# Optimization experiments

Measured on AMD Instinct MI355X. Metric: run time of the kernel, lower is better.

The kernel has to match this reference:

```python
import jax, jax.numpy as jnp
import numpy as np

H, C = 8, 32          # heads, per-head channels
N, E = 100000, 1600000
NEG_SLOPE = 0.2
LN_EPS = 1e-5


def layer_norm(x, g, b):
    mu = jnp.mean(x, axis=-1, keepdims=True)
    var = jnp.mean((x - mu) ** 2, axis=-1, keepdims=True)
    return (x - mu) * jax.lax.rsqrt(var + LN_EPS) * g + b


def setup_inputs() -> dict:
    key = jax.random.key(0)
    ks = jax.random.split(key, 8)
    x = jax.random.normal(ks[0], (N, C), dtype=jnp.float32)
    edge_index = jax.random.randint(ks[1], (2, E), 0, N, dtype=jnp.int64)
    s = 1.0 / np.sqrt(C)
    W_gat = jax.random.normal(ks[2], (C, H * C), dtype=jnp.float32) * s
    att_src = jax.random.normal(ks[3], (H, C), dtype=jnp.float32) * s
    att_dst = jax.random.normal(ks[4], (H, C), dtype=jnp.float32) * s
    bias_gat = jnp.zeros((C,), jnp.float32)
    w1 = jax.random.normal(ks[5], (C, 128), dtype=jnp.float32) * s
    b1 = jnp.zeros((128,), jnp.float32)
    w2 = jax.random.normal(ks[6], (128, C), dtype=jnp.float32) / np.sqrt(128)
    b2 = jnp.zeros((C,), jnp.float32)
    g1 = jnp.ones((C,), jnp.float32); be1 = jnp.zeros((C,), jnp.float32)
    g2 = jnp.ones((C,), jnp.float32); be2 = jnp.zeros((C,), jnp.float32)
    return dict(x=x, edge_index=edge_index, W_gat=W_gat, att_src=att_src,
                att_dst=att_dst, bias_gat=bias_gat, w1=w1, b1=b1, w2=w2,
                b2=b2, g1=g1, be1=be1, g2=g2, be2=be2)


def gat_conv(x, edge_index, W_gat, att_src, att_dst, bias_gat):
    n = x.shape[0]
    # add self loops (PyG default)
    loops = jnp.arange(n, dtype=edge_index.dtype)
    ei = jnp.concatenate([edge_index, jnp.stack([loops, loops])], axis=1)
    src, dst = ei[0], ei[1]
    xp = (x @ W_gat).reshape(n, H, C)                      # [N,H,C]
    a_src = jnp.einsum('nhc,hc->nh', xp, att_src)          # [N,H]
    a_dst = jnp.einsum('nhc,hc->nh', xp, att_dst)
    alpha = jax.nn.leaky_relu(a_src[src] + a_dst[dst], NEG_SLOPE)  # [E',H]
    # segment softmax over incoming edges of each dst node
    m = jax.ops.segment_max(alpha, dst, num_segments=n)
    ea = jnp.exp(alpha - m[dst])
    denom = jax.ops.segment_sum(ea, dst, num_segments=n)
    attn = ea / (denom[dst] + 1e-16)                       # [E',H]
    msg = xp[src] * attn[..., None]                        # [E',H,C]
    out = jax.ops.segment_sum(msg, dst, num_segments=n)    # [N,H,C]
    return out.mean(axis=1) + bias_gat                     # concat=False -> head mean


def reference(x, edge_index, W_gat, att_src, att_dst, bias_gat,
              w1, b1, w2, b2, g1, be1, g2, be2):
    h = gat_conv(x, edge_index, W_gat, att_src, att_dst, bias_gat)
    h = layer_norm(h + x, g1, be1)
    ff = jax.nn.relu(h @ w1 + b1) @ w2 + b2
    return layer_norm(ff + h, g2, be2)
```

## Files before the change

### kernel.cpp

```cpp
#include <hip/hip_runtime.h>
#include <hip/hip_fp16.h>
#include <stdint.h>

#define HH 8
#define CC 32
#define HC 256
#define FF 128
#define NEG 0.2f
#define LNEPS 1e-5f

typedef __attribute__((ext_vector_type(8))) short bf16x8;
typedef __attribute__((ext_vector_type(4))) float f32x4;
typedef unsigned short u16;

__device__ inline unsigned bf16r(float f) {
  unsigned u = __float_as_uint(f);
  return (u + 0x7fffu + ((u >> 16) & 1u)) >> 16;
}
__device__ inline float bflo(unsigned w) { return __uint_as_float(w << 16); }
__device__ inline float bfhi(unsigned w) { return __uint_as_float(w & 0xffff0000u); }
__device__ inline float leaky(float v) { return v >= 0.f ? v : NEG * v; }
__device__ inline float h2f(unsigned hbits) {
  return __half2float(__ushort_as_half((unsigned short)hbits));
}
__device__ inline u16 f2h(float f) {
  return __half_as_ushort(__float2half(f));
}
__device__ inline float ub0(unsigned w) { return (float)(w & 0xffu); }
__device__ inline float ub1(unsigned w) { return (float)((w >> 8) & 0xffu); }
__device__ inline float ub2(unsigned w) { return (float)((w >> 16) & 0xffu); }
__device__ inline float ub3(unsigned w) { return (float)(w >> 24); }

__global__ __launch_bounds__(256) void klayout(
    const float* __restrict__ W, const float* __restrict__ atts,
    const float* __restrict__ attd, const float* __restrict__ w1,
    const float* __restrict__ w2,
    u16* __restrict__ Wb, u16* __restrict__ Zb,
    u16* __restrict__ V1b, u16* __restrict__ V2b)
{
  int t = threadIdx.x;
  for (int i = t; i < 16 * 512; i += 256) {
    int j = i & 7, l = (i >> 3) & 63, nb = i >> 9;
    int k = 8 * (l >> 4) + j, c = 16 * nb + (l & 15);
    Wb[i] = (u16)bf16r(W[k * HC + c]);
  }
  for (int i = t; i < 8 * 512; i += 256) {
    int j = i & 7, l = (i >> 3) & 63, kb = i >> 9;
    int k = 32 * kb + 8 * (l >> 4) + j;
    int tc = l & 15;
    float v = 0.f;
    if (tc < 8)  { if ((k >> 5) == tc)     v = atts[tc * 32 + (k & 31)]; }
    else         { if ((k >> 5) == tc - 8) v = attd[(tc - 8) * 32 + (k & 31)]; }
    Zb[i] = (u16)bf16r(v);
  }
  for (int i = t; i < 8 * 512; i += 256) {
    int j = i & 7, l = (i >> 3) & 63, nb = i >> 9;
    int k = 8 * (l >> 4) + j, c = 16 * nb + (l & 15);
    V1b[i] = (u16)bf16r(w1[k * FF + c]);
  }
  for (int i = t; i < 8 * 512; i += 256) {
    int j = i & 7, l = (i >> 3) & 63, kn = i >> 9;
    int kb = kn >> 1, nb2 = kn & 1;
    int k = 32 * kb + 8 * (l >> 4) + j, c = 16 * nb2 + (l & 15);
    V2b[i] = (u16)bf16r(w2[k * CC + c]);
  }
}

__global__ __launch_bounds__(256) void khist(
    const int* __restrict__ ei, int e, int n,
    int* __restrict__ deg4, unsigned* __restrict__ dstr)
{
  int r = (int)blockIdx.x & 3;
  int* dr = deg4 + (size_t)r * n;
  int i = (int)blockIdx.x * 1024 + (int)threadIdx.x * 4;
  if (i >= e) return;
  const int* dst = ei + e;
  if (i + 3 < e) {
    int4 d4 = *(const int4*)(dst + i);
    unsigned r0 = (unsigned)atomicAdd(&dr[d4.x], 1);
    unsigned r1 = (unsigned)atomicAdd(&dr[d4.y], 1);
    unsigned r2 = (unsigned)atomicAdd(&dr[d4.z], 1);
    unsigned r3 = (unsigned)atomicAdd(&dr[d4.w], 1);
    uint4 o;
    o.x = (unsigned)d4.x | ((unsigned)r << 17) | (r0 << 19);
    o.y = (unsigned)d4.y | ((unsigned)r << 17) | (r1 << 19);
    o.z = (unsigned)d4.z | ((unsigned)r << 17) | (r2 << 19);
    o.w = (unsigned)d4.w | ((unsigned)r << 17) | (r3 << 19);
    *(uint4*)(dstr + i) = o;
  } else {
    for (int k = 0; k < 4 && i + k < e; ++k) {
      int d = dst[i + k];
      unsigned rr = (unsigned)atomicAdd(&dr[d], 1);
      dstr[i + k] = (unsigned)d | ((unsigned)r << 17) | (rr << 19);
    }
  }
}

__global__ __launch_bounds__(256) void k1c(
    const float* __restrict__ x, const u16* __restrict__ Wb,
    const u16* __restrict__ Zb,
    unsigned* __restrict__ xq8, unsigned* __restrict__ ascp,
    float* __restrict__ a_d, int n)
{
  __shared__ u16 lt[4][16 * 264];
  __shared__ float lsc[4][16][8];
  int wid = threadIdx.x >> 6, lane = threadIdx.x & 63;
  int q = lane & 15, g = lane >> 4;
  long node0 = (long)((int)blockIdx.x * 4 + wid) * 16;
  if (node0 + 16 > n) node0 = n - 16;
  u16* L = lt[wid];

  const float* xr = x + (node0 + q) * CC + 8 * g;
  float4 xa = *(const float4*)xr, xb = *(const float4*)(xr + 4);
  bf16x8 af;
  af[0] = (short)bf16r(xa.x); af[1] = (short)bf16r(xa.y);
  af[2] = (short)bf16r(xa.z); af[3] = (short)bf16r(xa.w);
  af[4] = (short)bf16r(xb.x); af[5] = (short)bf16r(xb.y);
  af[6] = (short)bf16r(xb.z); af[7] = (short)bf16r(xb.w);

#pragma unroll
  for (int nb = 0; nb < 16; ++nb) {
    bf16x8 bf = *(const bf16x8*)(Wb + nb * 512 + lane * 8);
    f32x4 acc = {0.f, 0.f, 0.f, 0.f};
    acc = __builtin_amdgcn_mfma_f32_16x16x32_bf16(af, bf, acc, 0, 0, 0);
    int col = 16 * nb + q;
#pragma unroll
    for (int r = 0; r < 4; ++r)
      L[(4 * g + r) * 264 + col] = (u16)bf16r(acc[r]);
  }
  __syncthreads();

  f32x4 az = {0.f, 0.f, 0.f, 0.f};
#pragma unroll
  for (int kb = 0; kb < 8; ++kb) {
    bf16x8 a2 = *(const bf16x8*)(L + q * 264 + kb * 32 + g * 8);
    bf16x8 zb = *(const bf16x8*)(Zb + kb * 512 + lane * 8);
    az = __builtin_amdgcn_mfma_f32_16x16x32_bf16(a2, zb, az, 0, 0, 0);
  }
  int hq = q & 7;
  u16* ascp16 = (u16*)ascp;
  if (q < 8) {
#pragma unroll
    for (int r = 0; r < 4; ++r)
      ascp16[((node0 + 4 * g + r) * HH + hq) * 2] = (u16)bf16r(az[r]);
  } else {
#pragma unroll
    for (int r = 0; r < 4; ++r)
      a_d[(node0 + 4 * g + r) * HH + hq] = az[r];
  }

#pragma unroll
  for (int t2 = 0; t2 < 2; ++t2) {
    int task = t2 * 64 + lane;
    int r = task >> 3, h = task & 7;
    const unsigned* p = (const unsigned*)(L + r * 264 + h * 32);
    float mx = 0.f;
#pragma unroll
    for (int i = 0; i < 16; ++i) {
      unsigned w = p[i];
      mx = fmaxf(mx, fmaxf(fabsf(bflo(w)), fabsf(bfhi(w))));
    }
    float rinv = (mx > 0.f) ? 127.f / mx : 0.f;
    ascp16[((node0 + r) * HH + h) * 2 + 1] = f2h(mx * (1.f / 127.f));
    lsc[wid][r][h] = rinv;
  }
  __syncthreads();

#pragma unroll
  for (int i = 0; i < 16; ++i) {
    int d = i * 64 + lane;
    int r = d >> 6, c = d & 63;
    int h = c >> 3;
    float rv = lsc[wid][r][h];
    const unsigned* p = (const unsigned*)(L + r * 264) + (c << 1);
    unsigned w0 = p[0], w1 = p[1];
    int q0 = __float2int_rn(bflo(w0) * rv);
    int q1 = __float2int_rn(bfhi(w0) * rv);
    int q2 = __float2int_rn(bflo(w1) * rv);
    int q3 = __float2int_rn(bfhi(w1) * rv);
    q0 = min(max(q0, -127), 127) + 128;
    q1 = min(max(q1, -127), 127) + 128;
    q2 = min(max(q2, -127), 127) + 128;
    q3 = min(max(q3, -127), 127) + 128;
    unsigned pk = (unsigned)q0 | ((unsigned)q1 << 8) |
                  ((unsigned)q2 << 16) | ((unsigned)q3 << 24);
    xq8[(node0 + r) * 64 + c] = pk;
  }
}

__global__ __launch_bounds__(256) void kscanA(const int* __restrict__ deg4,
                                              int* __restrict__ bsum, int n)
{
  __shared__ int ws[4];
  int t = threadIdx.x;
  int i = (int)blockIdx.x * 1024 + t * 4;
  int s = 0;
  if (i + 3 < n) {
#pragma unroll
    for (int r = 0; r < 4; ++r) {
      int4 v = *(const int4*)(deg4 + (size_t)r * n + i);
      s += v.x + v.y + v.z + v.w;
    }
  } else {
    for (int k = 0; k < 4 && i + k < n; ++k)
#pragma unroll
      for (int r = 0; r < 4; ++r) s += deg4[(size_t)r * n + i + k];
  }
#pragma unroll
  for (int mask = 1; mask < 64; mask <<= 1) s += __shfl_xor(s, mask);
  if ((t & 63) == 0) ws[t >> 6] = s;
  __syncthreads();
  if (t == 0) bsum[blockIdx.x] = ws[0] + ws[1] + ws[2] + ws[3];
}

__global__ __launch_bounds__(1024) void kscanB(int* __restrict__ bsum, int nb)
{
  __shared__ int wsum[16];
  int t = threadIdx.x, lane = t & 63, wid = t >> 6;
  int v = (t < nb) ? bsum[t] : 0;
  int s = v;
#pragma unroll
  for (int d = 1; d < 64; d <<= 1) { int tt = __shfl_up(s, d); if (lane >= d) s += tt; }
  if (lane == 63) wsum[wid] = s;
  __syncthreads();
  if (wid == 0) {
    int w = (lane < 16) ? wsum[lane] : 0;
#pragma unroll
    for (int d = 1; d < 16; d <<= 1) { int tt = __shfl_up(w, d); if (lane >= d) w += tt; }
    if (lane < 16) wsum[lane] = w;
  }
  __syncthreads();
  int excl = s - v + ((wid > 0) ? wsum[wid - 1] : 0);
  if (t < nb) bsum[t] = excl;
}

__global__ __launch_bounds__(256) void kscanC(const int* __restrict__ deg4,
                                              const int* __restrict__ bsum,
                                              int* __restrict__ rb,
                                              int* __restrict__ degt, int n)
{
  __shared__ int ws[4];
  int t = threadIdx.x, lane = t & 63, wid = t >> 6;
  int i = (int)blockIdx.x * 1024 + t * 4;
  int c0[4] = {0,0,0,0}, c1[4] = {0,0,0,0}, c2[4] = {0,0,0,0}, c3[4] = {0,0,0,0};
  if (i + 3 < n) {
    int4 v0 = *(const int4*)(deg4 + 0 * (size_t)n + i);
    int4 v1 = *(const int4*)(deg4 + 1 * (size_t)n + i);
    int4 v2 = *(const int4*)(deg4 + 2 * (size_t)n + i);
    int4 v3 = *(const int4*)(deg4 + 3 * (size_t)n + i);
    c0[0]=v0.x;c0[1]=v0.y;c0[2]=v0.z;c0[3]=v0.w;
    c1[0]=v1.x;c1[1]=v1.y;c1[2]=v1.z;c1[3]=v1.w;
    c2[0]=v2.x;c2[1]=v2.y;c2[2]=v2.z;c2[3]=v2.w;
    c3[0]=v3.x;c3[1]=v3.y;c3[2]=v3.z;c3[3]=v3.w;
  } else {
    for (int k = 0; k < 4 && i + k < n; ++k) {
      c0[k] = deg4[0 * (size_t)n + i + k];
      c1[k] = deg4[1 * (size_t)n + i + k];
      c2[k] = deg4[2 * (size_t)n + i + k];
      c3[k] = deg4[3 * (size_t)n + i + k];
    }
  }
  int tot[4];
#pragma unroll
  for (int k = 0; k < 4; ++k) tot[k] = c0[k] + c1[k] + c2[k] + c3[k];
  int tsum = tot[0] + tot[1] + tot[2] + tot[3];
  int s = tsum;
#pragma unroll
  for (int d = 1; d < 64; d <<= 1) { int tt = __shfl_up(s, d); if (lane >= d) s += tt; }
  if (lane == 63) ws[wid] = s;
  __syncthreads();
  if (t == 0) {
    int a = ws[0]; ws[0] = 0;
    int b = ws[1]; ws[1] = a; a += b;
    int c = ws[2]; ws[2] = a; a += c;
    ws[3] = a;
  }
  __syncthreads();
  int base = bsum[blockIdx.x] + ws[wid] + (s - tsum);
#pragma unroll
  for (int k = 0; k < 4; ++k) {
    if (i + k < n) {
      int b0 = base;
      rb[0 * (size_t)n + i + k] = b0;
      rb[1 * (size_t)n + i + k] = b0 + c0[k];
      rb[2 * (size_t)n + i + k] = b0 + c0[k] + c1[k];
      rb[3 * (size_t)n + i + k] = b0 + c0[k] + c1[k] + c2[k];
      degt[i + k] = tot[k];
    }
    base += tot[k];
  }
}

__global__ __launch_bounds__(256) void kscatter(
    const int* __restrict__ ei, const unsigned* __restrict__ dstr, int e,
    const int* __restrict__ rb, int* __restrict__ csr, int n)
{
  int oct = (int)blockIdx.x & 3;
  int nsub = (int)gridDim.x >> 2;
  int sub = (int)blockIdx.x >> 2;
  int nper = (n + 3) >> 2;
  int lo = oct * nper, hi = lo + nper;
  int stride = nsub << 10;
  for (int i = (sub * 256 + (int)threadIdx.x) * 4; i < e; i += stride) {
    if (i + 3 < e) {
      uint4 d4 = *(const uint4*)(dstr + i);
      int4 s4 = *(const int4*)(ei + i);
      int dx = d4.x & 0x1ffff, dy = d4.y & 0x1ffff,
          dz = d4.z & 0x1ffff, dw = d4.w & 0x1ffff;
      if (dx >= lo && dx < hi)
        csr[rb[(size_t)((d4.x >> 17) & 3) * n + dx] + (d4.x >> 19)] = s4.x;
      if (dy >= lo && dy < hi)
        csr[rb[(size_t)((d4.y >> 17) & 3) * n + dy] + (d4.y >> 19)] = s4.y;
      if (dz >= lo && dz < hi)
        csr[rb[(size_t)((d4.z >> 17) & 3) * n + dz] + (d4.z >> 19)] = s4.z;
      if (dw >= lo && dw < hi)
        csr[rb[(size_t)((d4.w >> 17) & 3) * n + dw] + (d4.w >> 19)] = s4.w;
    } else {
      for (int k = 0; k < 4 && i + k < e; ++k) {
        unsigned dv = dstr[i + k];
        int d = dv & 0x1ffff;
        if (d >= lo && d < hi)
          csr[rb[(size_t)((dv >> 17) & 3) * n + d] + (dv >> 19)] = ei[i + k];
      }
    }
  }
}

__global__ __launch_bounds__(256) void kagg(
    const int* __restrict__ csr, const int* __restrict__ offs,
    const int* __restrict__ degt,
    const unsigned* __restrict__ ascp, const float* __restrict__ a_d,
    const unsigned* __restrict__ xq8, float* __restrict__ og, int n)
{
  int lane = threadIdx.x & 63;
  int wid  = threadIdx.x >> 6;
  int base = ((int)blockIdx.x * 4 + wid) * 4;
  int eg = lane >> 3, ha = lane & 7;
  int hb = eg;
  int doff = hb * 8 + (lane & 7);

  for (int t = 0; t < 4; ++t) {
    int node = base + t;
    if (node >= n) return;
    int start = offs[node];
    int dg = degt[node];
    unsigned aw_self = ascp[(size_t)node * HH + ha];
    float ad_a  = a_d[(size_t)node * HH + ha];
    float aself = leaky(bflo(aw_self) + ad_a);

    float acc0 = 0.f, acc1 = 0.f, acc2 = 0.f, acc3 = 0.f;
    float dnA = 0.f, osA = 0.f;

    for (int j0 = 0; j0 < dg; j0 += 8) {
      int cnt = dg - j0; if (cnt > 8) cnt = 8;
      int idx = j0 + eg;
      int srcl = 0; float pw = 0.f;
      if (idx < dg) {
        srcl = csr[start + idx];
        unsigned av = ascp[(size_t)srcl * HH + ha];
        float al = leaky(bflo(av) + ad_a);
        float p  = __expf(al - aself);
        pw = p * h2f(av >> 16);
        dnA += p; osA += pw;
      }
      if (cnt == 8) {
#pragma unroll
        for (int j = 0; j < 8; ++j) {
          float wt = __shfl(pw, (j << 3) + hb);
          int s = __shfl(srcl, j << 3);
          unsigned w = xq8[(size_t)s * 64 + doff];
          acc0 = fmaf(ub0(w), wt, acc0);
          acc1 = fmaf(ub1(w), wt, acc1);
          acc2 = fmaf(ub2(w), wt, acc2);
          acc3 = fmaf(ub3(w), wt, acc3);
        }
      } else {
        for (int j = 0; j < cnt; ++j) {
          float wt = __shfl(pw, (j << 3) + hb);
          int s = __shfl(srcl, j << 3);
          unsigned w = xq8[(size_t)s * 64 + doff];
          acc0 = fmaf(ub0(w), wt, acc0);
          acc1 = fmaf(ub1(w), wt, acc1);
          acc2 = fmaf(ub2(w), wt, acc2);
          acc3 = fmaf(ub3(w), wt, acc3);
        }
      }
    }

    float dnH = dnA, osH = osA;
    dnH += __shfl_xor(dnH, 8);  osH += __shfl_xor(osH, 8);
    dnH += __shfl_xor(dnH, 16); osH += __shfl_xor(osH, 16);
    dnH += __shfl_xor(dnH, 32); osH += __shfl_xor(osH, 32);
    float dnB = __shfl(dnH, hb);
    float osB = __shfl(osH, hb);
    float scB = __shfl(h2f(aw_self >> 16), hb);

    {
      unsigned w = xq8[(size_t)node * 64 + doff];
      dnB += 1.f; osB += scB;
      acc0 = fmaf(ub0(w), scB, acc0);
      acc1 = fmaf(ub1(w), scB, acc1);
      acc2 = fmaf(ub2(w), scB, acc2);
      acc3 = fmaf(ub3(w), scB, acc3);
    }

    float corr = -128.f * osB;
    float inv = 0.125f / dnB;
    acc0 = (acc0 + corr) * inv;
    acc1 = (acc1 + corr) * inv;
    acc2 = (acc2 + corr) * inv;
    acc3 = (acc3 + corr) * inv;
#pragma unroll
    for (int mask = 8; mask < 64; mask <<= 1) {
      acc0 += __shfl_xor(acc0, mask);
      acc1 += __shfl_xor(acc1, mask);
      acc2 += __shfl_xor(acc2, mask);
      acc3 += __shfl_xor(acc3, mask);
    }
    if (lane < 8) {
      *(float4*)(og + (size_t)node * CC + lane * 4) =
        make_float4(acc0, acc1, acc2, acc3);
    }
  }
}

__global__ __launch_bounds__(256) void k5m(
    const float* __restrict__ og, const float* __restrict__ x,
    const float* __restrict__ bg,
    const u16* __restrict__ V1b, const u16* __restrict__ V2b,
    const float* __restrict__ b1, const float* __restrict__ b2,
    const float* __restrict__ g1, const float* __restrict__ be1,
    const float* __restrict__ g2, const float* __restrict__ be2,
    float* __restrict__ out, int n)
{
  __shared__ u16   lh[4][16 * 40];
  __shared__ u16   lf[4][16 * 136];
  __shared__ float lo[4][16 * 36];
  int wid = threadIdx.x >> 6, lane = threadIdx.x & 63;
  int q = lane & 15, g = lane >> 4;
  long node0 = (long)((int)blockIdx.x * 4 + wid) * 16;
  if (node0 + 16 > n) node0 = n - 16;
  u16* LH = lh[wid]; u16* LF = lf[wid]; float* LO = lo[wid];

  {
    int row = lane >> 2, off = (lane & 3) * 8;
    const float* o8 = og + (node0 + row) * CC + off;
    const float* x8 = x  + (node0 + row) * CC + off;
    float4 a0 = *(const float4*)o8, a1 = *(const float4*)(o8 + 4);
    float4 c0 = *(const float4*)x8, c1 = *(const float4*)(x8 + 4);
    float4 bg0 = *(const float4*)(bg + off), bg1 = *(const float4*)(bg + off + 4);
    float4 s0 = make_float4(a0.x + c0.x + bg0.x, a0.y + c0.y + bg0.y,
                            a0.z + c0.z + bg0.z, a0.w + c0.w + bg0.w);
    float4 s1 = make_float4(a1.x + c1.x + bg1.x, a1.y + c1.y + bg1.y,
                            a1.z + c1.z + bg1.z, a1.w + c1.w + bg1.w);
    *(float4*)(LO + row * 36 + off)     = s0;
    *(float4*)(LO + row * 36 + off + 4) = s1;
  }
  __syncthreads();

  float hv[32];
  if (lane < 16) {
#pragma unroll
    for (int i = 0; i < 8; ++i) {
      float4 t = *(const float4*)(LO + q * 36 + i * 4);
      hv[4*i] = t.x; hv[4*i+1] = t.y; hv[4*i+2] = t.z; hv[4*i+3] = t.w;
    }
    float mu = 0.f;
#pragma unroll
    for (int c = 0; c < 32; ++c) mu += hv[c];
    mu *= (1.f / 32.f);
    float var = 0.f;
#pragma unroll
    for (int c = 0; c < 32; ++c) { float t = hv[c] - mu; var = fmaf(t, t, var); }
    float rs = rsqrtf(var * (1.f / 32.f) + LNEPS);
#pragma unroll
    for (int c = 0; c < 32; ++c) hv[c] = (hv[c] - mu) * rs * g1[c] + be1[c];
    uint* dst = (uint*)(LH + q * 40);
#pragma unroll
    for (int i = 0; i < 16; ++i)
      dst[i] = bf16r(hv[2*i]) | (bf16r(hv[2*i+1]) << 16);
  }
  __syncthreads();

  bf16x8 ah = *(const bf16x8*)(LH + q * 40 + g * 8);
#pragma unroll
  for (int nb = 0; nb < 8; ++nb) {
    bf16x8 v1 = *(const bf16x8*)(V1b + nb * 512 + lane * 8);
    f32x4 acc = {0.f, 0.f, 0.f, 0.f};
    acc = __builtin_amdgcn_mfma_f32_16x16x32_bf16(ah, v1, acc, 0, 0, 0);
    int col = 16 * nb + q;
    float bias = b1[col];
#pragma unroll
    for (int r = 0; r < 4; ++r) {
      float f = fmaxf(acc[r] + bias, 0.f);
      LF[(4 * g + r) * 136 + col] = (u16)bf16r(f);
    }
  }
  __syncthreads();

  f32x4 a20 = {0.f, 0.f, 0.f, 0.f}, a21 = {0.f, 0.f, 0.f, 0.f};
#pragma unroll
  for (int kb = 0; kb < 4; ++kb) {
    bf16x8 af2 = *(const bf16x8*)(LF + q * 136 + kb * 32 + g * 8);
    bf16x8 v20 = *(const bf16x8*)(V2b + (kb * 2 + 0) * 512 + lane * 8);
    bf16x8 v21 = *(const bf16x8*)(V2b + (kb * 2 + 1) * 512 + lane * 8);
    a20 = __builtin_amdgcn_mfma_f32_16x16x32_bf16(af2, v20, a20, 0, 0, 0);
    a21 = __builtin_amdgcn_mfma_f32_16x16x32_bf16(af2, v21, a21, 0, 0, 0);
  }
  __syncthreads();
#pragma unroll
  for (int r = 0; r < 4; ++r) {
    LO[(4 * g + r) * 36 + q]      = a20[r];
    LO[(4 * g + r) * 36 + 16 + q] = a21[r];
  }
  __syncthreads();

  if (lane < 16) {
    float ov[32];
#pragma unroll
    for (int i = 0; i < 8; ++i) {
      float4 t = *(const float4*)(LO + q * 36 + i * 4);
      ov[4*i] = t.x; ov[4*i+1] = t.y; ov[4*i+2] = t.z; ov[4*i+3] = t.w;
    }
#pragma unroll
    for (int c = 0; c < 32; ++c) ov[c] += b2[c] + hv[c];
    float mu2 = 0.f;
#pragma unroll
    for (int c = 0; c < 32; ++c) mu2 += ov[c];
    mu2 *= (1.f / 32.f);
    float var2 = 0.f;
#pragma unroll
    for (int c = 0; c < 32; ++c) { float t = ov[c] - mu2; var2 = fmaf(t, t, var2); }
    float rs2 = rsqrtf(var2 * (1.f / 32.f) + LNEPS);
    float* op = out + (node0 + q) * CC;
#pragma unroll
    for (int i = 0; i < 8; ++i) {
      float4 o;
      o.x = (ov[4*i]   - mu2) * rs2 * g2[4*i]   + be2[4*i];
      o.y = (ov[4*i+1] - mu2) * rs2 * g2[4*i+1] + be2[4*i+1];
      o.z = (ov[4*i+2] - mu2) * rs2 * g2[4*i+2] + be2[4*i+2];
      o.w = (ov[4*i+3] - mu2) * rs2 * g2[4*i+3] + be2[4*i+3];
      *(float4*)(op + i * 4) = o;
    }
  }
}

extern "C" void kernel_launch(void* const* d_in, const int* in_sizes, int n_in,
                              void* d_out, int out_size, void* d_ws, size_t ws_size,
                              hipStream_t stream)
{
  const float* x    = (const float*)d_in[0];
  const int*   ei   = (const int*)d_in[1];
  const float* W    = (const float*)d_in[2];
  const float* atts = (const float*)d_in[3];
  const float* attd = (const float*)d_in[4];
  const float* bg   = (const float*)d_in[5];
  const float* w1   = (const float*)d_in[6];
  const float* b1   = (const float*)d_in[7];
  const float* w2   = (const float*)d_in[8];
  const float* b2   = (const float*)d_in[9];
  const float* g1   = (const float*)d_in[10];
  const float* be1  = (const float*)d_in[11];
  const float* g2   = (const float*)d_in[12];
  const float* be2  = (const float*)d_in[13];

  int n = in_sizes[0] / CC;
  int e = in_sizes[1] / 2;

  uint8_t* ws = (uint8_t*)d_ws;
  size_t o = 0;
  unsigned* xq8 = (unsigned*)(ws + o); o += (size_t)n * 256;
  unsigned* ascp = (unsigned*)(ws + o); o += (size_t)n * HH * 4;
  float* a_d = (float*)(ws + o); o += (size_t)n * HH * 4;
  float* og  = (float*)(ws + o); o += (size_t)n * CC * 4;
  int* deg4   = (int*)(ws + o); o += (size_t)n * 4 * 4;
  int* rb     = (int*)(ws + o); o += (size_t)n * 4 * 4;
  int* degt   = (int*)(ws + o); o += (size_t)n * 4;
  unsigned* dstr = (unsigned*)(ws + o); o += (size_t)e * 4;
  int* csr    = (int*)(ws + o); o += (size_t)e * 4;
  int* bsum   = (int*)(ws + o); o += 4096;
  u16* Wb  = (u16*)(ws + o); o += 16 * 512 * 2;
  u16* Zb  = (u16*)(ws + o); o += 8 * 512 * 2;
  u16* V1b = (u16*)(ws + o); o += 8 * 512 * 2;
  u16* V2b = (u16*)(ws + o); o += 8 * 512 * 2;

  (void)hipMemsetAsync(deg4, 0, (size_t)n * 4 * 4, stream);

  int nwaves = (n + 15) / 16;
  int nbc   = (nwaves + 3) / 4;
  int nb_e4 = (e + 1023) / 1024;
  int nb_s  = (n + 1023) / 1024;
  int nb_ag = (n + 15) / 16;

  khist   <<<nb_e4, 256, 0, stream>>>(ei, e, n, deg4, dstr);
  klayout <<<1, 256, 0, stream>>>(W, atts, attd, w1, w2, Wb, Zb, V1b, V2b);
  k1c     <<<nbc, 256, 0, stream>>>(x, Wb, Zb, xq8, ascp, a_d, n);
  kscanA  <<<nb_s, 256, 0, stream>>>(deg4, bsum, n);
  kscanB  <<<1, 1024, 0, stream>>>(bsum, nb_s);
  kscanC  <<<nb_s, 256, 0, stream>>>(deg4, bsum, rb, degt, n);
  kscatter<<<512, 256, 0, stream>>>(ei, dstr, e, rb, csr, n);
  kagg    <<<nb_ag, 256, 0, stream>>>(csr, rb, degt, ascp, a_d, xq8, og, n);
  k5m     <<<nbc, 256, 0, stream>>>(og, x, bg, V1b, V2b, b1, b2, g1, be1, g2, be2,
                                    (float*)d_out, n);
}
```

Before: 253.3 us.

## Aggregate raw x per head and apply W_gat after aggregation

Instead of quantizing and gathering the projected 256-wide features per source node, the aggregation now gathers an int8-quantized copy of raw x (32 values per node) and accumulates per-head weighted sums of x. The per-head projection through W_gat (folded with the head mean) is then applied in the final kernel as an MFMA over the 256-wide bf16 aggregate. This uses linearity to shrink the gathered row from 256 to 32 bytes, cutting random-gather traffic in the edge loop. In exchange it writes and reads a larger 512-byte-per-node intermediate, adds matmul work to the last kernel, and changes where quantization error enters.

```diff
diff --git a/kernel.cpp b/kernel.cpp
--- a/kernel.cpp
+++ b/kernel.cpp
@@ -36,7 +36,7 @@
     const float* __restrict__ attd, const float* __restrict__ w1,
     const float* __restrict__ w2,
     u16* __restrict__ Wb, u16* __restrict__ Zb,
-    u16* __restrict__ V1b, u16* __restrict__ V2b)
+    u16* __restrict__ V1b, u16* __restrict__ V2b, u16* __restrict__ WSb)
 {
   int t = threadIdx.x;
   for (int i = t; i < 16 * 512; i += 256) {
@@ -63,6 +63,14 @@
     int kb = kn >> 1, nb2 = kn & 1;
     int k = 32 * kb + 8 * (l >> 4) + j, c = 16 * nb2 + (l & 15);
     V2b[i] = (u16)bf16r(w2[k * CC + c]);
+  }
+  for (int i = t; i < 16 * 512; i += 256) {
+    int j = i & 7, l = (i >> 3) & 63, kn = i >> 9;
+    int kb = kn >> 1, nb2 = kn & 1;
+    int krow = kb * 32 + 8 * (l >> 4) + j;
+    int h = krow >> 5, kk = krow & 31;
+    int c = 16 * nb2 + (l & 15);
+    WSb[i] = (u16)bf16r(W[kk * HC + h * 32 + c]);
   }
 }
 
@@ -99,16 +107,16 @@
 __global__ __launch_bounds__(256) void k1c(
     const float* __restrict__ x, const u16* __restrict__ Wb,
     const u16* __restrict__ Zb,
-    unsigned* __restrict__ xq8, unsigned* __restrict__ ascp,
+    unsigned* __restrict__ xqx, unsigned* __restrict__ ascp,
     float* __restrict__ a_d, int n)
 {
   __shared__ u16 lt[4][16 * 264];
-  __shared__ float lsc[4][16][8];
   int wid = threadIdx.x >> 6, lane = threadIdx.x & 63;
   int q = lane & 15, g = lane >> 4;
   long node0 = (long)((int)blockIdx.x * 4 + wid) * 16;
   if (node0 + 16 > n) node0 = n - 16;
   u16* L = lt[wid];
+  u16* ascp16 = (u16*)ascp;
 
   const float* xr = x + (node0 + q) * CC + 8 * g;
   float4 xa = *(const float4*)xr, xb = *(const float4*)(xr + 4);
@@ -118,6 +126,29 @@
   af[4] = (short)bf16r(xb.x); af[5] = (short)bf16r(xb.y);
   af[6] = (short)bf16r(xb.z); af[7] = (short)bf16r(xb.w);
 
+  float mx = fmaxf(fmaxf(fmaxf(fabsf(xa.x), fabsf(xa.y)), fmaxf(fabsf(xa.z), fabsf(xa.w))),
+                   fmaxf(fmaxf(fabsf(xb.x), fabsf(xb.y)), fmaxf(fabsf(xb.z), fabsf(xb.w))));
+  mx = fmaxf(mx, __shfl_xor(mx, 16));
+  mx = fmaxf(mx, __shfl_xor(mx, 32));
+  float rinv = (mx > 0.f) ? 127.f / mx : 0.f;
+  u16 sch = f2h(mx * (1.f / 127.f));
+  ascp16[((node0 + q) * HH + 2 * g) * 2 + 1]     = sch;
+  ascp16[((node0 + q) * HH + 2 * g + 1) * 2 + 1] = sch;
+  {
+    int q0 = min(max(__float2int_rn(xa.x * rinv), -127), 127) + 128;
+    int q1 = min(max(__float2int_rn(xa.y * rinv), -127), 127) + 128;
+    int q2 = min(max(__float2int_rn(xa.z * rinv), -127), 127) + 128;
+    int q3 = min(max(__float2int_rn(xa.w * rinv), -127), 127) + 128;
+    int q4 = min(max(__float2int_rn(xb.x * rinv), -127), 127) + 128;
+    int q5 = min(max(__float2int_rn(xb.y * rinv), -127), 127) + 128;
+    int q6 = min(max(__float2int_rn(xb.z * rinv), -127), 127) + 128;
+    int q7 = min(max(__float2int_rn(xb.w * rinv), -127), 127) + 128;
+    uint2 pk;
+    pk.x = (unsigned)q0 | ((unsigned)q1 << 8) | ((unsigned)q2 << 16) | ((unsigned)q3 << 24);
+    pk.y = (unsigned)q4 | ((unsigned)q5 << 8) | ((unsigned)q6 << 16) | ((unsigned)q7 << 24);
+    *(uint2*)(xqx + (node0 + q) * 8 + 2 * g) = pk;
+  }
+
 #pragma unroll
   for (int nb = 0; nb < 16; ++nb) {
     bf16x8 bf = *(const bf16x8*)(Wb + nb * 512 + lane * 8);
@@ -138,7 +169,6 @@
     az = __builtin_amdgcn_mfma_f32_16x16x32_bf16(a2, zb, az, 0, 0, 0);
   }
   int hq = q & 7;
-  u16* ascp16 = (u16*)ascp;
   if (q < 8) {
 #pragma unroll
     for (int r = 0; r < 4; ++r)
@@ -147,44 +177,6 @@
 #pragma unroll
     for (int r = 0; r < 4; ++r)
       a_d[(node0 + 4 * g + r) * HH + hq] = az[r];
-  }
-
-#pragma unroll
-  for (int t2 = 0; t2 < 2; ++t2) {
-    int task = t2 * 64 + lane;
-    int r = task >> 3, h = task & 7;
-    const unsigned* p = (const unsigned*)(L + r * 264 + h * 32);
-    float mx = 0.f;
-#pragma unroll
-    for (int i = 0; i < 16; ++i) {
-      unsigned w = p[i];
-      mx = fmaxf(mx, fmaxf(fabsf(bflo(w)), fabsf(bfhi(w))));
-    }
-    float rinv = (mx > 0.f) ? 127.f / mx : 0.f;
-    ascp16[((node0 + r) * HH + h) * 2 + 1] = f2h(mx * (1.f / 127.f));
-    lsc[wid][r][h] = rinv;
-  }
-  __syncthreads();
-
-#pragma unroll
-  for (int i = 0; i < 16; ++i) {
-    int d = i * 64 + lane;
-    int r = d >> 6, c = d & 63;
-    int h = c >> 3;
-    float rv = lsc[wid][r][h];
-    const unsigned* p = (const unsigned*)(L + r * 264) + (c << 1);
-    unsigned w0 = p[0], w1 = p[1];
-    int q0 = __float2int_rn(bflo(w0) * rv);
-    int q1 = __float2int_rn(bfhi(w0) * rv);
-    int q2 = __float2int_rn(bflo(w1) * rv);
-    int q3 = __float2int_rn(bfhi(w1) * rv);
-    q0 = min(max(q0, -127), 127) + 128;
-    q1 = min(max(q1, -127), 127) + 128;
-    q2 = min(max(q2, -127), 127) + 128;
-    q3 = min(max(q3, -127), 127) + 128;
-    unsigned pk = (unsigned)q0 | ((unsigned)q1 << 8) |
-                  ((unsigned)q2 << 16) | ((unsigned)q3 << 24);
-    xq8[(node0 + r) * 64 + c] = pk;
   }
 }
 
@@ -330,14 +322,14 @@
     const int* __restrict__ csr, const int* __restrict__ offs,
     const int* __restrict__ degt,
     const unsigned* __restrict__ ascp, const float* __restrict__ a_d,
-    const unsigned* __restrict__ xq8, float* __restrict__ og, int n)
+    const unsigned* __restrict__ xqx, unsigned* __restrict__ agg32, int n)
 {
   int lane = threadIdx.x & 63;
   int wid  = threadIdx.x >> 6;
   int base = ((int)blockIdx.x * 4 + wid) * 4;
   int eg = lane >> 3, ha = lane & 7;
   int hb = eg;
-  int doff = hb * 8 + (lane & 7);
+  int c4 = lane & 7;
 
   for (int t = 0; t < 4; ++t) {
     int node = base + t;
@@ -368,7 +360,7 @@
         for (int j = 0; j < 8; ++j) {
           float wt = __shfl(pw, (j << 3) + hb);
           int s = __shfl(srcl, j << 3);
-          unsigned w = xq8[(size_t)s * 64 + doff];
+          unsigned w = xqx[(size_t)s * 8 + c4];
           acc0 = fmaf(ub0(w), wt, acc0);
           acc1 = fmaf(ub1(w), wt, acc1);
           acc2 = fmaf(ub2(w), wt, acc2);
@@ -378,7 +370,7 @@
         for (int j = 0; j < cnt; ++j) {
           float wt = __shfl(pw, (j << 3) + hb);
           int s = __shfl(srcl, j << 3);
-          unsigned w = xq8[(size_t)s * 64 + doff];
+          unsigned w = xqx[(size_t)s * 8 + c4];
           acc0 = fmaf(ub0(w), wt, acc0);
           acc1 = fmaf(ub1(w), wt, acc1);
           acc2 = fmaf(ub2(w), wt, acc2);
@@ -396,7 +388,7 @@
     float scB = __shfl(h2f(aw_self >> 16), hb);
 
     {
-      unsigned w = xq8[(size_t)node * 64 + doff];
+      unsigned w = xqx[(size_t)node * 8 + c4];
       dnB += 1.f; osB += scB;
       acc0 = fmaf(ub0(w), scB, acc0);
       acc1 = fmaf(ub1(w), scB, acc1);
@@ -410,23 +402,16 @@
     acc1 = (acc1 + corr) * inv;
     acc2 = (acc2 + corr) * inv;
     acc3 = (acc3 + corr) * inv;
-#pragma unroll
-    for (int mask = 8; mask < 64; mask <<= 1) {
-      acc0 += __shfl_xor(acc0, mask);
-      acc1 += __shfl_xor(acc1, mask);
-      acc2 += __shfl_xor(acc2, mask);
-      acc3 += __shfl_xor(acc3, mask);
-    }
-    if (lane < 8) {
-      *(float4*)(og + (size_t)node * CC + lane * 4) =
-        make_float4(acc0, acc1, acc2, acc3);
-    }
+    uint2 pk;
+    pk.x = bf16r(acc0) | (bf16r(acc1) << 16);
+    pk.y = bf16r(acc2) | (bf16r(acc3) << 16);
+    *(uint2*)(agg32 + (size_t)node * 128 + hb * 16 + c4 * 2) = pk;
   }
 }
 
 __global__ __launch_bounds__(256) void k5m(
-    const float* __restrict__ og, const float* __restrict__ x,
-    const float* __restrict__ bg,
+    const u16* __restrict__ agg16, const float* __restrict__ x,
+    const float* __restrict__ bg, const u16* __restrict__ WSb,
     const u16* __restrict__ V1b, const u16* __restrict__ V2b,
     const float* __restrict__ b1, const float* __restrict__ b2,
     const float* __restrict__ g1, const float* __restrict__ be1,
@@ -444,17 +429,31 @@
 
   {
     int row = lane >> 2, off = (lane & 3) * 8;
-    const float* o8 = og + (node0 + row) * CC + off;
-    const float* x8 = x  + (node0 + row) * CC + off;
-    float4 a0 = *(const float4*)o8, a1 = *(const float4*)(o8 + 4);
+    const float* x8 = x + (node0 + row) * CC + off;
     float4 c0 = *(const float4*)x8, c1 = *(const float4*)(x8 + 4);
     float4 bg0 = *(const float4*)(bg + off), bg1 = *(const float4*)(bg + off + 4);
-    float4 s0 = make_float4(a0.x + c0.x + bg0.x, a0.y + c0.y + bg0.y,
-                            a0.z + c0.z + bg0.z, a0.w + c0.w + bg0.w);
-    float4 s1 = make_float4(a1.x + c1.x + bg1.x, a1.y + c1.y + bg1.y,
-                            a1.z + c1.z + bg1.z, a1.w + c1.w + bg1.w);
+    float4 s0 = make_float4(c0.x + bg0.x, c0.y + bg0.y, c0.z + bg0.z, c0.w + bg0.w);
+    float4 s1 = make_float4(c1.x + bg1.x, c1.y + bg1.y, c1.z + bg1.z, c1.w + bg1.w);
     *(float4*)(LO + row * 36 + off)     = s0;
     *(float4*)(LO + row * 36 + off + 4) = s1;
+  }
+  __syncthreads();
+
+  {
+    f32x4 a20 = {0.f, 0.f, 0.f, 0.f}, a21 = {0.f, 0.f, 0.f, 0.f};
+#pragma unroll
+    for (int kb = 0; kb < 8; ++kb) {
+      bf16x8 af = *(const bf16x8*)(agg16 + (node0 + q) * 256 + kb * 32 + g * 8);
+      bf16x8 w0 = *(const bf16x8*)(WSb + (kb * 2 + 0) * 512 + lane * 8);
+      bf16x8 w1v = *(const bf16x8*)(WSb + (kb * 2 + 1) * 512 + lane * 8);
+      a20 = __builtin_amdgcn_mfma_f32_16x16x32_bf16(af, w0, a20, 0, 0, 0);
+      a21 = __builtin_amdgcn_mfma_f32_16x16x32_bf16(af, w1v, a21, 0, 0, 0);
+    }
+#pragma unroll
+    for (int r = 0; r < 4; ++r) {
+      LO[(4 * g + r) * 36 + q]      += a20[r];
+      LO[(4 * g + r) * 36 + 16 + q] += a21[r];
+    }
   }
   __syncthreads();
 
@@ -569,10 +568,10 @@
 
   uint8_t* ws = (uint8_t*)d_ws;
   size_t o = 0;
-  unsigned* xq8 = (unsigned*)(ws + o); o += (size_t)n * 256;
+  unsigned* xqx = (unsigned*)(ws + o); o += (size_t)n * 32;
   unsigned* ascp = (unsigned*)(ws + o); o += (size_t)n * HH * 4;
   float* a_d = (float*)(ws + o); o += (size_t)n * HH * 4;
-  float* og  = (float*)(ws + o); o += (size_t)n * CC * 4;
+  unsigned* agg32 = (unsigned*)(ws + o); o += (size_t)n * 512;
   int* deg4   = (int*)(ws + o); o += (size_t)n * 4 * 4;
   int* rb     = (int*)(ws + o); o += (size_t)n * 4 * 4;
   int* degt   = (int*)(ws + o); o += (size_t)n * 4;
@@ -583,6 +582,7 @@
   u16* Zb  = (u16*)(ws + o); o += 8 * 512 * 2;
   u16* V1b = (u16*)(ws + o); o += 8 * 512 * 2;
   u16* V2b = (u16*)(ws + o); o += 8 * 512 * 2;
+  u16* WSb = (u16*)(ws + o); o += 16 * 512 * 2;
 
   (void)hipMemsetAsync(deg4, 0, (size_t)n * 4 * 4, stream);
 
@@ -593,13 +593,13 @@
   int nb_ag = (n + 15) / 16;
 
   khist   <<<nb_e4, 256, 0, stream>>>(ei, e, n, deg4, dstr);
-  klayout <<<1, 256, 0, stream>>>(W, atts, attd, w1, w2, Wb, Zb, V1b, V2b);
-  k1c     <<<nbc, 256, 0, stream>>>(x, Wb, Zb, xq8, ascp, a_d, n);
+  klayout <<<1, 256, 0, stream>>>(W, atts, attd, w1, w2, Wb, Zb, V1b, V2b, WSb);
+  k1c     <<<nbc, 256, 0, stream>>>(x, Wb, Zb, xqx, ascp, a_d, n);
   kscanA  <<<nb_s, 256, 0, stream>>>(deg4, bsum, n);
   kscanB  <<<1, 1024, 0, stream>>>(bsum, nb_s);
   kscanC  <<<nb_s, 256, 0, stream>>>(deg4, bsum, rb, degt, n);
   kscatter<<<512, 256, 0, stream>>>(ei, dstr, e, rb, csr, n);
-  kagg    <<<nb_ag, 256, 0, stream>>>(csr, rb, degt, ascp, a_d, xq8, og, n);
-  k5m     <<<nbc, 256, 0, stream>>>(og, x, bg, V1b, V2b, b1, b2, g1, be1, g2, be2,
-                                    (float*)d_out, n);
-}
+  kagg    <<<nb_ag, 256, 0, stream>>>(csr, rb, degt, ascp, a_d, xqx, agg32, n);
+  k5m     <<<nbc, 256, 0, stream>>>((const u16*)agg32, x, bg, WSb, V1b, V2b,
+                                    b1, b2, g1, be1, g2, be2, (float*)d_out, n);
+}
```

After: 246.0 us. 2.9% less time.
